# Performance work log

Measured on AMD Instinct MI355X. Metric: run time of the kernel, lower is better.

Reference implementation:

```python
import jax, jax.numpy as jnp
import numpy as np
from jax import lax

LAM = 1.0   # risk.distance calls wasserstein with lam=1
ITS = 20    # and its=20
EPS_K = 1e-6


def setup_inputs() -> dict:
    key = jax.random.key(0)
    k1, k2 = jax.random.split(key)
    N, S, D = 4096, 32, 128
    X_ls = jax.random.normal(k1, (N, S, D), dtype=jnp.float32)
    t = jax.random.randint(k2, (N,), 0, 2).astype(jnp.int32)
    return {"X_ls": X_ls, "t": t}


def _pdist2sq(X, Y):
    # squared Euclidean distance between all pairs: [nt, nc]
    C = -2.0 * (X @ Y.T)
    nx = jnp.sum(jnp.square(X), axis=1, keepdims=True)   # [nt,1]
    ny = jnp.sum(jnp.square(Y), axis=1, keepdims=True)   # [nc,1]
    return C + ny.T + nx


def _sinkhorn_step(Xt, Xc, p, lam, its):
    # Xt: [nt, d], Xc: [nc, d]  -> scalar 2*sum(T*Mt)
    nt = jnp.float32(Xt.shape[0])
    nc = jnp.float32(Xc.shape[0])
    M = _pdist2sq(Xt, Xc)                                   # [nt, nc]
    delta = lax.stop_gradient(jnp.max(M))
    eff_lam = lax.stop_gradient(lam / jnp.mean(M))
    # augmented cost matrix Mt: [nt+1, nc+1]
    row = delta * jnp.ones((1, M.shape[1]), M.dtype)
    col = jnp.concatenate([delta * jnp.ones((M.shape[0], 1), M.dtype),
                           jnp.zeros((1, 1), M.dtype)], axis=0)
    Mt = jnp.concatenate([jnp.concatenate([M, row], axis=0), col], axis=1)
    # marginals a: [nt+1,1], b: [nc+1,1]
    a = jnp.concatenate([(p / nt) * jnp.ones((Xt.shape[0], 1), M.dtype),
                         (1.0 - p) * jnp.ones((1, 1), M.dtype)], axis=0)
    b = jnp.concatenate([((1.0 - p) / nc) * jnp.ones((Xc.shape[0], 1), M.dtype),
                         p * jnp.ones((1, 1), M.dtype)], axis=0)
    K = jnp.exp(-eff_lam * Mt) + EPS_K
    ainvK = K / a
    def body(i, u):
        # u^T K -> transpose -> K^T u : [nc+1,1]
        return 1.0 / (ainvK @ (b / (K.T @ u)))
    u = lax.fori_loop(0, its, body, a)
    v = b / (K.T @ u)                                       # [nc+1,1]
    T = u * (v.T * K)                                       # [nt+1, nc+1]
    T = lax.stop_gradient(T)                                # backpropT=False
    return 2.0 * jnp.sum(T * Mt)


def _wasserstein(X_ls, t, lam=LAM, its=ITS):
    # Data-dependent split on treatment (concrete, eager) — matches tf.where+gather.
    t_np = np.asarray(t)
    it_idx = np.nonzero(t_np > 0)[0]
    ic_idx = np.nonzero(t_np < 1)[0]
    p = jnp.float32(t_np.astype(np.float32).mean())          # p_t = np.mean(t)
    Xt_all = jnp.transpose(X_ls[it_idx], (1, 0, 2))          # [S, nt, d]
    Xc_all = jnp.transpose(X_ls[ic_idx], (1, 0, 2))          # [S, nc, d]
    per_step = jax.vmap(lambda Xt, Xc: _sinkhorn_step(Xt, Xc, p, lam, its))
    return jnp.sum(per_step(Xt_all, Xc_all))                 # sum over timesteps


def reference(X_ls, t):
    return _wasserstein(X_ls, t)
```

## Files before the change

kernel.cpp:

```cpp
#include <hip/hip_runtime.h>
#include <stdint.h>

typedef unsigned char u8;
typedef unsigned short u16;
typedef uint32_t u32;

#define NTOT 4096
#define SS   32
#define DD   128
#define EPSK 1e-6f
#define NITER 20
#define CAPC 4460544u
#define LDC_FIT 2304
#define WSTR 2432
#define SU_OFF 2308
#define UNT_OFF 2309
#define BPT 16

typedef __attribute__((ext_vector_type(8))) short short8;
typedef __attribute__((ext_vector_type(4))) float f32x4;
typedef __attribute__((ext_vector_type(2))) float f32x2;

__device__ __forceinline__ float bf2f(u16 h){ return __uint_as_float(((u32)h) << 16); }
__device__ __forceinline__ u16 f2bf(float f){
  u32 u = __float_as_uint(f);
  u += 0x7fffu + ((u >> 16) & 1u);
  return (u16)(u >> 16);
}
__device__ __forceinline__ int invpermc(int cp){
  return (cp & ~63) | ((cp & 3) << 4) | ((cp >> 2) & 15);
}

__global__ __launch_bounds__(1024) void k_compact(const int* __restrict__ t,
    int* __restrict__ itidx, int* __restrict__ icidx, int* __restrict__ meta,
    float* __restrict__ fmeta)
{
  __shared__ int sc[1024];
  int tid = threadIdx.x;
  int e0 = tid * 4;
  int tv[4]; int c = 0;
  #pragma unroll
  for (int e = 0; e < 4; e++){ tv[e] = t[e0 + e]; c += (tv[e] > 0) ? 1 : 0; }
  sc[tid] = c;
  __syncthreads();
  for (int off = 1; off < 1024; off <<= 1){
    int v = sc[tid];
    int add = (tid >= off) ? sc[tid - off] : 0;
    __syncthreads();
    sc[tid] = v + add;
    __syncthreads();
  }
  int incl = sc[tid];
  int excl = incl - c;
  int oT = excl, oC = e0 - excl;
  #pragma unroll
  for (int e = 0; e < 4; e++){
    if (tv[e] > 0) itidx[oT++] = e0 + e;
    else           icidx[oC++] = e0 + e;
  }
  if (tid == 1023){
    meta[0] = incl; meta[1] = NTOT - incl;
    fmeta[0] = (float)incl / (float)NTOT;
  }
}

__global__ void k_zero(float* __restrict__ p, int n)
{
  int i = blockIdx.x * 256 + threadIdx.x;
  if (i < n) p[i] = 0.f;
}

__global__ void k_vinit(const float* __restrict__ fmeta, float* __restrict__ w0)
{
  if (threadIdx.x == 0){
    float p = fmeta[0];
    float* w = w0 + (size_t)blockIdx.x * WSTR;
    w[SU_OFF]  = p;
    w[UNT_OFF] = 1.0f - p;
  }
}

__global__ __launch_bounds__(256) void k_pack(const float* __restrict__ X,
    const int* __restrict__ itidx, const int* __restrict__ icidx,
    const int* __restrict__ meta, u16* __restrict__ XT, u16* __restrict__ XC,
    float* __restrict__ nxT, float* __restrict__ nxC, int ts0)
{
  int r = blockIdx.x * 256 + threadIdx.x;
  int isC = blockIdx.y;
  int z = blockIdx.z;
  int s = ts0 + z;
  int n = isC ? meta[1] : meta[0];
  if (r >= n) return;
  int idx = isC ? icidx[r] : itidx[r];
  const float4* src = (const float4*)(X + ((size_t)idx * SS + s) * DD);
  u16* dst = (isC ? XC : XT) + ((size_t)z * NTOT + r) * DD;
  float nrm = 0.f;
  #pragma unroll
  for (int q = 0; q < 32; q++){
    float4 v = src[q];
    nrm += v.x*v.x + v.y*v.y + v.z*v.z + v.w*v.w;
    u32 lo = (u32)f2bf(v.x) | ((u32)f2bf(v.y) << 16);
    u32 hi = (u32)f2bf(v.z) | ((u32)f2bf(v.w) << 16);
    uint2 pk; pk.x = lo; pk.y = hi;
    ((uint2*)dst)[q] = pk;
  }
  (isC ? nxC : nxT)[z * NTOT + r] = nrm;
}

__global__ __launch_bounds__(256) void k_stats(const u16* __restrict__ XT,
    const u16* __restrict__ XC, const float* __restrict__ nxT, const float* __restrict__ nxC,
    const int* __restrict__ meta, float* __restrict__ gsx, float* __restrict__ gsn)
{
  int side = blockIdx.y, z = blockIdx.z;
  int n = side ? meta[1] : meta[0];
  int chunk = (n + 7) >> 3;
  int r0 = blockIdx.x * chunk;
  int r1 = min(r0 + chunk, n);
  const u16* B = (side ? XC : XT) + (size_t)z * NTOT * DD;
  int tid = threadIdx.x;
  int d = tid & 127, half = tid >> 7;
  float sx = 0.f;
  for (int r = r0 + half; r < r1; r += 2) sx += bf2f(B[(size_t)r * DD + d]);
  __shared__ float sp[256];
  sp[tid] = sx;
  __syncthreads();
  if (tid < 128) unsafeAtomicAdd(&gsx[(size_t)(z*2+side)*128 + tid], sp[tid] + sp[tid+128]);
  const float* nrm = (side ? nxC : nxT) + (size_t)z * NTOT;
  float sn = 0.f;
  for (int r = r0 + tid; r < r1; r += 256) sn += nrm[r];
  #pragma unroll
  for (int o = 32; o; o >>= 1) sn += __shfl_xor(sn, o);
  __syncthreads();
  if ((tid & 63) == 0) sp[tid >> 6] = sn;
  __syncthreads();
  if (tid == 0) unsafeAtomicAdd(&gsn[z*2+side], sp[0]+sp[1]+sp[2]+sp[3]);
}

__global__ void k_lam(const float* __restrict__ gsx, const float* __restrict__ gsn,
                      const int* __restrict__ meta, float* __restrict__ stats)
{
  int z = blockIdx.x, tid = threadIdx.x;
  float d = gsx[(size_t)(z*2)*128 + tid] * gsx[(size_t)(z*2+1)*128 + tid];
  #pragma unroll
  for (int o = 32; o; o >>= 1) d += __shfl_xor(d, o);
  __shared__ float rr[2];
  if ((tid & 63) == 0) rr[tid >> 6] = d;
  __syncthreads();
  if (tid == 0){
    float nt = (float)meta[0], nc = (float)meta[1];
    float msum = nc * gsn[z*2] + nt * gsn[z*2+1] - 2.f * (rr[0] + rr[1]);
    stats[z*8+0] = nt * nc / msum;
    stats[z*8+1] = msum / (nt * nc);
  }
}

#define LDA2 72
__global__ __launch_bounds__(256) void k_gemm(const u16* __restrict__ XT,
    const u16* __restrict__ XC, const float* __restrict__ nxT, const float* __restrict__ nxC,
    const int* __restrict__ meta, const float* __restrict__ fmeta,
    float* __restrict__ stats, u8* __restrict__ Kc, float* __restrict__ w0base)
{
  int nt = meta[0], nc = meta[1];
  if (nt > LDC_FIT || nc > LDC_FIT) return;
  int bx = blockIdx.x, by = blockIdx.y, z = blockIdx.z;
  if (by * 128 >= nt || bx * 128 >= nc) return;
  __shared__ __align__(16) u16 As[128 * LDA2];
  __shared__ __align__(16) u16 Bs[128 * LDA2];
  __shared__ float watile[256];
  int tid = threadIdx.x;
  int wid = tid >> 6, lane = tid & 63;
  int wm = (wid >> 1) * 64, wn = (wid & 1) * 64;
  int lrow = lane & 15, lquad = lane >> 4;

  f32x4 acc[4][4];
  #pragma unroll
  for (int i = 0; i < 4; i++){
    #pragma unroll
    for (int j = 0; j < 4; j++){
      acc[i][j][0]=0.f; acc[i][j][1]=0.f; acc[i][j][2]=0.f; acc[i][j][3]=0.f;
    }
  }

  int r = tid & 127;
  int isB = tid >> 7;
  int g = (isB ? bx : by) * 128 + r;
  int lim = isB ? nc : nt;
  const u16* srcbase = (isB ? XC : XT) + ((size_t)z * NTOT + g) * DD;
  u16* dl = (isB ? Bs : As) + r * LDA2;

  for (int kh = 0; kh < 2; kh++){
    __syncthreads();
    if (g < lim){
      const uint4* src = (const uint4*)(srcbase + kh * 64);
      #pragma unroll
      for (int q = 0; q < 8; q++) ((uint4*)dl)[q] = src[q];
    } else {
      uint4 zz; zz.x=0; zz.y=0; zz.z=0; zz.w=0;
      #pragma unroll
      for (int q = 0; q < 8; q++) ((uint4*)dl)[q] = zz;
    }
    __syncthreads();
    #pragma unroll
    for (int ks = 0; ks < 2; ks++){
      int koff = ks * 32 + lquad * 8;
      short8 af[4], bfr[4];
      #pragma unroll
      for (int i = 0; i < 4; i++) af[i]  = *(const short8*)(As + (wm + i*16 + lrow) * LDA2 + koff);
      #pragma unroll
      for (int j = 0; j < 4; j++) bfr[j] = *(const short8*)(Bs + (wn + j*16 + lrow) * LDA2 + koff);
      #pragma unroll
      for (int i = 0; i < 4; i++){
        #pragma unroll
        for (int j = 0; j < 4; j++){
          acc[i][j] = __builtin_amdgcn_mfma_f32_16x16x32_bf16(af[i], bfr[j], acc[i][j], 0, 0, 0);
        }
      }
    }
  }

  int ldc = (nc + 127) & ~127;
  float lam = stats[z*8+0];
  float p = fmeta[0];
  float a0 = p / (float)nt;
  const float* nxTr = nxT + (size_t)z * NTOT;
  const float* nxCr = nxC + (size_t)z * NTOT;
  u8* Kz = Kc + (size_t)z * CAPC;

  float nyv[4]; bool jin[4];
  #pragma unroll
  for (int j = 0; j < 4; j++){
    int gj = bx*128 + wn + j*16 + lrow;
    jin[j] = gj < nc;
    nyv[j] = jin[j] ? nxCr[gj] : 0.f;
  }
  float vmax = 0.f;
  float colsum[4] = {0.f, 0.f, 0.f, 0.f};
  size_t cbase = (size_t)(bx*128 + wn + lrow*4);
  #pragma unroll
  for (int i = 0; i < 4; i++){
    #pragma unroll
    for (int rr2 = 0; rr2 < 4; rr2++){
      int gi = by*128 + wm + i*16 + lquad*4 + rr2;
      bool iin = gi < nt;
      float nxv = iin ? nxTr[gi] : 0.f;
      float cv[4];
      #pragma unroll
      for (int j = 0; j < 4; j++){
        float m = nxv + nyv[j] - 2.0f * acc[i][j][rr2];
        cv[j] = __expf(-lam * m);
        if (iin && jin[j]){ vmax = fmaxf(vmax, m); colsum[j] += cv[j]; }
      }
      u32 pk = (u32)__builtin_amdgcn_cvt_pk_fp8_f32(cv[0], cv[1], 0, false);
      pk = (u32)__builtin_amdgcn_cvt_pk_fp8_f32(cv[2], cv[3], (int)pk, true);
      if (iin) *(u32*)(Kz + (size_t)gi * ldc + cbase) = pk;
    }
  }
  #pragma unroll
  for (int j = 0; j < 4; j++){
    colsum[j] += __shfl_xor(colsum[j], 16);
    colsum[j] += __shfl_xor(colsum[j], 32);
  }
  if (lane < 16){
    #pragma unroll
    for (int j = 0; j < 4; j++) watile[wid * 64 + j*16 + lrow] = colsum[j];
  }
  #pragma unroll
  for (int o = 32; o; o >>= 1) vmax = fmaxf(vmax, __shfl_xor(vmax, o));
  if (lane == 0) atomicMax((int*)stats + z*8 + 2, __float_as_int(vmax));
  __syncthreads();
  if (tid < 128){
    int gj = bx*128 + tid;
    if (gj < nc){
      float v = (tid < 64) ? (watile[tid] + watile[128 + tid])
                           : (watile[64 + (tid-64)] + watile[192 + (tid-64)]);
      unsafeAtomicAdd(w0base + (size_t)z * WSTR + gj, v * a0);
    }
  }
}

__global__ __launch_bounds__(256, 2) void k_iter(const u8* __restrict__ Kc,
    const float* __restrict__ wprev, float* __restrict__ wnext,
    float* __restrict__ ubuf, const int* __restrict__ meta,
    const float* __restrict__ fmeta, const float* __restrict__ stats, int writeU)
{
  __shared__ __align__(16) float zl[LDC_FIT];
  __shared__ __align__(16) float watw[4 * LDC_FIT];
  __shared__ float red[4];
  int nt = meta[0], nc = meta[1];
  if (nt > LDC_FIT || nc > LDC_FIT) return;
  int ldc = (nc + 127) & ~127;
  int z = blockIdx.y, b = blockIdx.x;
  int tid = threadIdx.x, wid = tid >> 6, lane = tid & 63;
  float p = fmeta[0];
  float b0 = (1.0f - p) / (float)nc;
  float a0 = p / (float)nt;
  float lam = stats[z*8+0];
  float delta = stats[z*8+2];
  float kc = __expf(-lam * delta);
  float kce = kc + EPSK;
  const float* wp = wprev + (size_t)z * WSTR;
  float* wnx = wnext + (size_t)z * WSTR;
  float SU = wp[SU_OFF], UNT = wp[UNT_OFF];
  float wext = EPSK * (SU + UNT) + kc * UNT;
  float wnc = kce * SU + (1.0f + EPSK) * UNT;
  float znc = p / wnc;

  float zp = 0.f;
  for (int cp = tid; cp < ldc; cp += 256){
    int c = invpermc(cp);
    float v = 0.f;
    if (c < nc) v = b0 * __builtin_amdgcn_rcpf(wp[c] + wext);
    zl[cp] = v;
    zp += v;
  }
  #pragma unroll
  for (int o = 32; o; o >>= 1) zp += __shfl_xor(zp, o);
  if (lane == 0) red[wid] = zp;
  __syncthreads();
  float Z = red[0] + red[1] + red[2] + red[3];
  float dotX = EPSK * Z + kce * znc;
  float untN = (1.0f - p) / (kce * Z + (1.0f + EPSK) * znc);

  int cb0 = lane * 16;
  float zv[48];
  #pragma unroll
  for (int s = 0; s < 3; s++){
    int cb = s*1024 + cb0;
    if (cb < ldc){
      #pragma unroll
      for (int q = 0; q < 4; q++){
        float4 t4 = *(const float4*)(zl + cb + q*4);
        zv[s*16+q*4+0]=t4.x; zv[s*16+q*4+1]=t4.y; zv[s*16+q*4+2]=t4.z; zv[s*16+q*4+3]=t4.w;
      }
    } else {
      #pragma unroll
      for (int k = 0; k < 16; k++) zv[s*16+k] = 0.f;
    }
  }

  float wacc[48];
  #pragma unroll
  for (int k = 0; k < 48; k++) wacc[k] = 0.f;
  float rsum = 0.f;

  int rpb = (nt + BPT - 1) / BPT;
  int r0 = b * rpb, r1 = min(r0 + rpb, nt);
  const u8* Kz = Kc + (size_t)z * CAPC;

  for (int r = r0 + wid; r < r1; r += 4){
    const u8* Kr = Kz + (size_t)r * ldc;
    uint4 kq[3];
    #pragma unroll
    for (int s = 0; s < 3; s++){
      int cb = s*1024 + cb0;
      if (cb < ldc) kq[s] = *(const uint4*)(Kr + cb);
      else { kq[s].x=0u; kq[s].y=0u; kq[s].z=0u; kq[s].w=0u; }
    }
    float kd[48];
    #pragma unroll
    for (int s = 0; s < 3; s++){
      u32 wd[4] = {kq[s].x, kq[s].y, kq[s].z, kq[s].w};
      #pragma unroll
      for (int q = 0; q < 4; q++){
        f32x2 d0 = __builtin_amdgcn_cvt_pk_f32_fp8((int)wd[q], false);
        f32x2 d1 = __builtin_amdgcn_cvt_pk_f32_fp8((int)wd[q], true);
        kd[s*16+q*4+0] = d0.x; kd[s*16+q*4+1] = d0.y;
        kd[s*16+q*4+2] = d1.x; kd[s*16+q*4+3] = d1.y;
      }
    }
    float dot = 0.f;
    #pragma unroll
    for (int k = 0; k < 48; k++) dot = fmaf(kd[k], zv[k], dot);
    #pragma unroll
    for (int o = 32; o; o >>= 1) dot += __shfl_xor(dot, o);
    float uv = a0 * __builtin_amdgcn_rcpf(dot + dotX);
    rsum += uv;
    if (writeU && lane == 0) ubuf[(size_t)z * WSTR + r] = uv;
    #pragma unroll
    for (int k = 0; k < 48; k++) wacc[k] = fmaf(kd[k], uv, wacc[k]);
  }
  #pragma unroll
  for (int s = 0; s < 3; s++){
    int cb = s*1024 + cb0;
    if (cb < ldc){
      #pragma unroll
      for (int q = 0; q < 4; q++)
        *(float4*)(watw + (size_t)wid * LDC_FIT + cb + q*4) =
            make_float4(wacc[s*16+q*4+0], wacc[s*16+q*4+1], wacc[s*16+q*4+2], wacc[s*16+q*4+3]);
    }
  }
  if (lane == 0) unsafeAtomicAdd(wnx + SU_OFF, rsum);
  if (b == 0 && tid == 0) wnx[UNT_OFF] = untN;
  __syncthreads();
  for (int cp = tid; cp < ldc; cp += 256){
    int c = invpermc(cp);
    if (c < nc){
      float v = watw[cp] + watw[LDC_FIT + cp] + watw[2*LDC_FIT + cp] + watw[3*LDC_FIT + cp];
      unsafeAtomicAdd(wnx + c, v);
    }
  }
}

__global__ __launch_bounds__(256, 2) void k_fin(const u8* __restrict__ Kc,
    const float* __restrict__ wprev, const float* __restrict__ ubuf,
    const int* __restrict__ meta, const float* __restrict__ fmeta,
    const float* __restrict__ stats, float* __restrict__ tsacc, int ts0)
{
  __shared__ __align__(16) float zl[LDC_FIT];
  __shared__ float red[4];
  int nt = meta[0], nc = meta[1];
  if (nt > LDC_FIT || nc > LDC_FIT) return;
  int ldc = (nc + 127) & ~127;
  int z = blockIdx.y, b = blockIdx.x;
  int tid = threadIdx.x, wid = tid >> 6, lane = tid & 63;
  float p = fmeta[0];
  float b0 = (1.0f - p) / (float)nc;
  float lam = stats[z*8+0];
  float invlam = stats[z*8+1];
  float delta = stats[z*8+2];
  float kc = __expf(-lam * delta);
  float kce = kc + EPSK;
  const float* wp = wprev + (size_t)z * WSTR;
  float SU = wp[SU_OFF], UNT = wp[UNT_OFF];
  float wext = EPSK * (SU + UNT) + kc * UNT;
  float wnc = kce * SU + (1.0f + EPSK) * UNT;
  float znc = p / wnc;

  float zp = 0.f;
  for (int cp = tid; cp < ldc; cp += 256){
    int c = invpermc(cp);
    float v = 0.f;
    if (c < nc) v = b0 * __builtin_amdgcn_rcpf(wp[c] + wext);
    zl[cp] = v;
    zp += v;
  }
  #pragma unroll
  for (int o = 32; o; o >>= 1) zp += __shfl_xor(zp, o);
  if (lane == 0) red[wid] = zp;
  __syncthreads();
  float Z = red[0] + red[1] + red[2] + red[3];

  int cb0 = lane * 16;
  float zv[48];
  #pragma unroll
  for (int s = 0; s < 3; s++){
    int cb = s*1024 + cb0;
    if (cb < ldc){
      #pragma unroll
      for (int q = 0; q < 4; q++){
        float4 t4 = *(const float4*)(zl + cb + q*4);
        zv[s*16+q*4+0]=t4.x; zv[s*16+q*4+1]=t4.y; zv[s*16+q*4+2]=t4.z; zv[s*16+q*4+3]=t4.w;
      }
    } else {
      #pragma unroll
      for (int k = 0; k < 16; k++) zv[s*16+k] = 0.f;
    }
  }

  int rpb = (nt + BPT - 1) / BPT;
  int r0 = b * rpb, r1 = min(r0 + rpb, nt);
  const u8* Kz = Kc + (size_t)z * CAPC;
  float wsum = 0.f;

  for (int r = r0 + wid; r < r1; r += 4){
    const u8* Kr = Kz + (size_t)r * ldc;
    float inner = 0.f;
    #pragma unroll
    for (int s = 0; s < 3; s++){
      int cb = s*1024 + cb0;
      if (cb < ldc){
        uint4 kq = *(const uint4*)(Kr + cb);
        u32 wd[4] = {kq.x, kq.y, kq.z, kq.w};
        #pragma unroll
        for (int q = 0; q < 4; q++){
          f32x2 d0 = __builtin_amdgcn_cvt_pk_f32_fp8((int)wd[q], false);
          f32x2 d1 = __builtin_amdgcn_cvt_pk_f32_fp8((int)wd[q], true);
          float c0 = d0.x, c1 = d0.y, c2 = d1.x, c3 = d1.y;
          int k0 = s*16+q*4;
          inner += (c0 + EPSK) * zv[k0+0] * __logf(fmaxf(c0, 1e-4f));
          inner += (c1 + EPSK) * zv[k0+1] * __logf(fmaxf(c1, 1e-4f));
          inner += (c2 + EPSK) * zv[k0+2] * __logf(fmaxf(c2, 1e-4f));
          inner += (c3 + EPSK) * zv[k0+3] * __logf(fmaxf(c3, 1e-4f));
        }
      }
    }
    #pragma unroll
    for (int o = 32; o; o >>= 1) inner += __shfl_xor(inner, o);
    wsum += ubuf[(size_t)z * WSTR + r] * inner;
  }
  if (lane == 0) unsafeAtomicAdd(tsacc + ts0 + z, -invlam * wsum);
  if (b == 0 && tid == 0){
    float aug = delta * kce * (UNT * Z + SU * znc);
    unsafeAtomicAdd(tsacc + ts0 + z, aug);
  }
}

__global__ void k_out(const float* __restrict__ tsacc, float* __restrict__ out)
{
  if (threadIdx.x == 0){
    float s = 0.f;
    for (int i = 0; i < SS; i++) s += tsacc[i];
    out[0] = 2.0f * s;
  }
}

extern "C" void kernel_launch(void* const* d_in, const int* in_sizes, int n_in,
                              void* d_out, int out_size, void* d_ws, size_t ws_size,
                              hipStream_t stream)
{
  const float* X = (const float*)d_in[0];
  const int* t = (const int*)d_in[1];

  const size_t PER_TS = 6810000u;
  const size_t FIXED  = 262144u;
  int TSG = 1;
  if (ws_size > FIXED + PER_TS){
    size_t g = (ws_size - FIXED) / PER_TS;
    TSG = (g > SS) ? SS : (int)g;
  }

  char* pp = (char*)d_ws;
  auto alloc = [&](size_t bytes) -> void* {
    void* r = (void*)pp;
    pp += (bytes + 255) & ~(size_t)255;
    return r;
  };
  u8*    Kbuf  = (u8*)alloc((size_t)TSG * CAPC);
  u16*   XT    = (u16*)alloc((size_t)TSG * NTOT * DD * 2);
  u16*   XC    = (u16*)alloc((size_t)TSG * NTOT * DD * 2);
  float* nxT   = (float*)alloc((size_t)TSG * NTOT * 4);
  float* nxC   = (float*)alloc((size_t)TSG * NTOT * 4);
  float* wbuf  = (float*)alloc((size_t)(NITER + 1) * TSG * WSTR * 4);
  float* ubuf  = (float*)alloc((size_t)TSG * WSTR * 4);
  float* auxf  = (float*)alloc((size_t)TSG * 272 * 4);
  int*   itidx = (int*)alloc(NTOT * 4);
  int*   icidx = (int*)alloc(NTOT * 4);
  int*   meta  = (int*)alloc(256);
  float* fmeta = (float*)alloc(256);
  float* tsacc = (float*)alloc(256);

  float* gsx   = auxf;
  float* gsn   = auxf + (size_t)TSG*256;
  float* stats = gsn + (size_t)TSG*2;
  const int auxn = TSG * 266;
  const int wn  = (NITER + 1) * TSG * WSTR;

  k_zero<<<1, 256, 0, stream>>>(tsacc, 64);
  k_compact<<<1, 1024, 0, stream>>>(t, itidx, icidx, meta, fmeta);

  for (int ts0 = 0; ts0 < SS; ts0 += TSG){
    int cnt = SS - ts0; if (cnt > TSG) cnt = TSG;

    k_zero<<<(auxn + 255)/256, 256, 0, stream>>>(auxf, auxn);
    k_zero<<<(wn + 255)/256, 256, 0, stream>>>(wbuf, wn);
    k_vinit<<<cnt, 64, 0, stream>>>(fmeta, wbuf);
    k_pack<<<dim3(16, 2, cnt), 256, 0, stream>>>(X, itidx, icidx, meta, XT, XC, nxT, nxC, ts0);
    k_stats<<<dim3(8, 2, cnt), 256, 0, stream>>>(XT, XC, nxT, nxC, meta, gsx, gsn);
    k_lam<<<cnt, 128, 0, stream>>>(gsx, gsn, meta, stats);
    k_gemm<<<dim3(18, 18, cnt), 256, 0, stream>>>(XT, XC, nxT, nxC, meta, fmeta, stats, Kbuf, wbuf);

    for (int it = 0; it < NITER; it++){
      k_iter<<<dim3(BPT, cnt), 256, 0, stream>>>(Kbuf,
          wbuf + (size_t)it * TSG * WSTR,
          wbuf + (size_t)(it + 1) * TSG * WSTR,
          ubuf, meta, fmeta, stats, (it == NITER - 1) ? 1 : 0);
    }
    k_fin<<<dim3(BPT, cnt), 256, 0, stream>>>(Kbuf,
        wbuf + (size_t)NITER * TSG * WSTR, ubuf, meta, fmeta, stats, tsacc, ts0);
  }
  k_out<<<1, 64, 0, stream>>>(tsacc, (float*)d_out);
}
```

Measured before the change: 1.248 ms.

## Prefetch K rows, cut iter LDS with shared atomics, raise occupancy and grid

The Sinkhorn iteration and final kernels now software-prefetch the next row's fp8 K values while processing the current one. They re-decode K instead of keeping 48 decoded floats live, and split dot products into four accumulators. k_iter replaces its four per-wave LDS partial buffers with a single buffer updated by LDS atomics, which shrinks shared memory so occupancy can rise to 3 blocks per CU. BPT grows from 16 to 24 blocks per timestep. k_gemm stages the norm vectors in LDS and requests 4 blocks per CU. The costs are LDS atomic contention and the extra fp8 decode work.

```diff
diff --git a/kernel.cpp b/kernel.cpp
--- a/kernel.cpp
+++ b/kernel.cpp
@@ -15,7 +15,7 @@
 #define WSTR 2432
 #define SU_OFF 2308
 #define UNT_OFF 2309
-#define BPT 16
+#define BPT 24
 
 typedef __attribute__((ext_vector_type(8))) short short8;
 typedef __attribute__((ext_vector_type(4))) float f32x4;
@@ -29,6 +29,15 @@
 }
 __device__ __forceinline__ int invpermc(int cp){
   return (cp & ~63) | ((cp & 3) << 4) | ((cp >> 2) & 15);
+}
+__device__ __forceinline__ void dec16(uint4 kq, float* kd){
+  u32 wd[4] = {kq.x, kq.y, kq.z, kq.w};
+  #pragma unroll
+  for (int q = 0; q < 4; q++){
+    f32x2 d0 = __builtin_amdgcn_cvt_pk_f32_fp8((int)wd[q], false);
+    f32x2 d1 = __builtin_amdgcn_cvt_pk_f32_fp8((int)wd[q], true);
+    kd[q*4+0] = d0.x; kd[q*4+1] = d0.y; kd[q*4+2] = d1.x; kd[q*4+3] = d1.y;
+  }
 }
 
 __global__ __launch_bounds__(1024) void k_compact(const int* __restrict__ t,
@@ -155,7 +164,7 @@
 }
 
 #define LDA2 72
-__global__ __launch_bounds__(256) void k_gemm(const u16* __restrict__ XT,
+__global__ __launch_bounds__(256, 4) void k_gemm(const u16* __restrict__ XT,
     const u16* __restrict__ XC, const float* __restrict__ nxT, const float* __restrict__ nxC,
     const int* __restrict__ meta, const float* __restrict__ fmeta,
     float* __restrict__ stats, u8* __restrict__ Kc, float* __restrict__ w0base)
@@ -167,10 +176,20 @@
   __shared__ __align__(16) u16 As[128 * LDA2];
   __shared__ __align__(16) u16 Bs[128 * LDA2];
   __shared__ float watile[256];
+  __shared__ float nxs[128];
+  __shared__ float nys[128];
   int tid = threadIdx.x;
   int wid = tid >> 6, lane = tid & 63;
   int wm = (wid >> 1) * 64, wn = (wid & 1) * 64;
   int lrow = lane & 15, lquad = lane >> 4;
+
+  if (tid < 128){
+    int gi = by*128 + tid;
+    nxs[tid] = (gi < nt) ? nxT[(size_t)z * NTOT + gi] : 0.f;
+  } else {
+    int gj = bx*128 + (tid - 128);
+    nys[tid - 128] = (gj < nc) ? nxC[(size_t)z * NTOT + gj] : 0.f;
+  }
 
   f32x4 acc[4][4];
   #pragma unroll
@@ -222,16 +241,14 @@
   float lam = stats[z*8+0];
   float p = fmeta[0];
   float a0 = p / (float)nt;
-  const float* nxTr = nxT + (size_t)z * NTOT;
-  const float* nxCr = nxC + (size_t)z * NTOT;
   u8* Kz = Kc + (size_t)z * CAPC;
 
   float nyv[4]; bool jin[4];
   #pragma unroll
   for (int j = 0; j < 4; j++){
-    int gj = bx*128 + wn + j*16 + lrow;
-    jin[j] = gj < nc;
-    nyv[j] = jin[j] ? nxCr[gj] : 0.f;
+    int lcol = wn + j*16 + lrow;
+    jin[j] = (bx*128 + lcol) < nc;
+    nyv[j] = nys[lcol];
   }
   float vmax = 0.f;
   float colsum[4] = {0.f, 0.f, 0.f, 0.f};
@@ -240,9 +257,10 @@
   for (int i = 0; i < 4; i++){
     #pragma unroll
     for (int rr2 = 0; rr2 < 4; rr2++){
-      int gi = by*128 + wm + i*16 + lquad*4 + rr2;
+      int lr = wm + i*16 + lquad*4 + rr2;
+      int gi = by*128 + lr;
       bool iin = gi < nt;
-      float nxv = iin ? nxTr[gi] : 0.f;
+      float nxv = nxs[lr];
       float cv[4];
       #pragma unroll
       for (int j = 0; j < 4; j++){
@@ -278,13 +296,13 @@
   }
 }
 
-__global__ __launch_bounds__(256, 2) void k_iter(const u8* __restrict__ Kc,
+__global__ __launch_bounds__(256, 3) void k_iter(const u8* __restrict__ Kc,
     const float* __restrict__ wprev, float* __restrict__ wnext,
     float* __restrict__ ubuf, const int* __restrict__ meta,
     const float* __restrict__ fmeta, const float* __restrict__ stats, int writeU)
 {
   __shared__ __align__(16) float zl[LDC_FIT];
-  __shared__ __align__(16) float watw[4 * LDC_FIT];
+  __shared__ float watw[LDC_FIT];
   __shared__ float red[4];
   int nt = meta[0], nc = meta[1];
   if (nt > LDC_FIT || nc > LDC_FIT) return;
@@ -311,6 +329,7 @@
     float v = 0.f;
     if (c < nc) v = b0 * __builtin_amdgcn_rcpf(wp[c] + wext);
     zl[cp] = v;
+    watw[cp] = 0.f;
     zp += v;
   }
   #pragma unroll
@@ -346,47 +365,55 @@
   int rpb = (nt + BPT - 1) / BPT;
   int r0 = b * rpb, r1 = min(r0 + rpb, nt);
   const u8* Kz = Kc + (size_t)z * CAPC;
-
-  for (int r = r0 + wid; r < r1; r += 4){
+  uint4 zq; zq.x=0u; zq.y=0u; zq.z=0u; zq.w=0u;
+
+  int r = r0 + wid;
+  uint4 cur[3] = {zq, zq, zq};
+  if (r < r1){
     const u8* Kr = Kz + (size_t)r * ldc;
-    uint4 kq[3];
+    cur[0] = *(const uint4*)(Kr + cb0);
+    if (1024 + cb0 < ldc) cur[1] = *(const uint4*)(Kr + 1024 + cb0);
+    if (2048 + cb0 < ldc) cur[2] = *(const uint4*)(Kr + 2048 + cb0);
+  }
+  while (r < r1){
+    int rn = r + 4;
+    uint4 nxt[3] = {zq, zq, zq};
+    if (rn < r1){
+      const u8* Krn = Kz + (size_t)rn * ldc;
+      nxt[0] = *(const uint4*)(Krn + cb0);
+      if (1024 + cb0 < ldc) nxt[1] = *(const uint4*)(Krn + 1024 + cb0);
+      if (2048 + cb0 < ldc) nxt[2] = *(const uint4*)(Krn + 2048 + cb0);
+    }
+    float d4[4] = {0.f, 0.f, 0.f, 0.f};
     #pragma unroll
     for (int s = 0; s < 3; s++){
-      int cb = s*1024 + cb0;
-      if (cb < ldc) kq[s] = *(const uint4*)(Kr + cb);
-      else { kq[s].x=0u; kq[s].y=0u; kq[s].z=0u; kq[s].w=0u; }
-    }
-    float kd[48];
-    #pragma unroll
-    for (int s = 0; s < 3; s++){
-      u32 wd[4] = {kq[s].x, kq[s].y, kq[s].z, kq[s].w};
-      #pragma unroll
-      for (int q = 0; q < 4; q++){
-        f32x2 d0 = __builtin_amdgcn_cvt_pk_f32_fp8((int)wd[q], false);
-        f32x2 d1 = __builtin_amdgcn_cvt_pk_f32_fp8((int)wd[q], true);
-        kd[s*16+q*4+0] = d0.x; kd[s*16+q*4+1] = d0.y;
-        kd[s*16+q*4+2] = d1.x; kd[s*16+q*4+3] = d1.y;
-      }
-    }
-    float dot = 0.f;
-    #pragma unroll
-    for (int k = 0; k < 48; k++) dot = fmaf(kd[k], zv[k], dot);
+      float kd[16];
+      dec16(cur[s], kd);
+      #pragma unroll
+      for (int k = 0; k < 16; k++) d4[k & 3] = fmaf(kd[k], zv[s*16+k], d4[k & 3]);
+    }
+    float dot = (d4[0] + d4[1]) + (d4[2] + d4[3]);
     #pragma unroll
     for (int o = 32; o; o >>= 1) dot += __shfl_xor(dot, o);
     float uv = a0 * __builtin_amdgcn_rcpf(dot + dotX);
     rsum += uv;
     if (writeU && lane == 0) ubuf[(size_t)z * WSTR + r] = uv;
     #pragma unroll
-    for (int k = 0; k < 48; k++) wacc[k] = fmaf(kd[k], uv, wacc[k]);
+    for (int s = 0; s < 3; s++){
+      float kd[16];
+      dec16(cur[s], kd);
+      #pragma unroll
+      for (int k = 0; k < 16; k++) wacc[s*16+k] = fmaf(kd[k], uv, wacc[s*16+k]);
+    }
+    cur[0] = nxt[0]; cur[1] = nxt[1]; cur[2] = nxt[2];
+    r = rn;
   }
   #pragma unroll
   for (int s = 0; s < 3; s++){
     int cb = s*1024 + cb0;
     if (cb < ldc){
       #pragma unroll
-      for (int q = 0; q < 4; q++)
-        *(float4*)(watw + (size_t)wid * LDC_FIT + cb + q*4) =
-            make_float4(wacc[s*16+q*4+0], wacc[s*16+q*4+1], wacc[s*16+q*4+2], wacc[s*16+q*4+3]);
+      for (int k = 0; k < 16; k++) atomicAdd(&watw[cb + k], wacc[s*16+k]);
     }
   }
   if (lane == 0) unsafeAtomicAdd(wnx + SU_OFF, rsum);
@@ -394,14 +421,11 @@
   __syncthreads();
   for (int cp = tid; cp < ldc; cp += 256){
     int c = invpermc(cp);
-    if (c < nc){
-      float v = watw[cp] + watw[LDC_FIT + cp] + watw[2*LDC_FIT + cp] + watw[3*LDC_FIT + cp];
-      unsafeAtomicAdd(wnx + c, v);
-    }
-  }
-}
-
-__global__ __launch_bounds__(256, 2) void k_fin(const u8* __restrict__ Kc,
+    if (c < nc) unsafeAtomicAdd(wnx + c, watw[cp]);
+  }
+}
+
+__global__ __launch_bounds__(256, 3) void k_fin(const u8* __restrict__ Kc,
     const float* __restrict__ wprev, const float* __restrict__ ubuf,
     const int* __restrict__ meta, const float* __restrict__ fmeta,
     const float* __restrict__ stats, float* __restrict__ tsacc, int ts0)
@@ -461,32 +485,42 @@
   int r0 = b * rpb, r1 = min(r0 + rpb, nt);
   const u8* Kz = Kc + (size_t)z * CAPC;
   float wsum = 0.f;
-
-  for (int r = r0 + wid; r < r1; r += 4){
+  uint4 zq; zq.x=0u; zq.y=0u; zq.z=0u; zq.w=0u;
+
+  int r = r0 + wid;
+  uint4 cur[3] = {zq, zq, zq};
+  if (r < r1){
     const u8* Kr = Kz + (size_t)r * ldc;
-    float inner = 0.f;
+    cur[0] = *(const uint4*)(Kr + cb0);
+    if (1024 + cb0 < ldc) cur[1] = *(const uint4*)(Kr + 1024 + cb0);
+    if (2048 + cb0 < ldc) cur[2] = *(const uint4*)(Kr + 2048 + cb0);
+  }
+  while (r < r1){
+    int rn = r + 4;
+    uint4 nxt[3] = {zq, zq, zq};
+    if (rn < r1){
+      const u8* Krn = Kz + (size_t)rn * ldc;
+      nxt[0] = *(const uint4*)(Krn + cb0);
+      if (1024 + cb0 < ldc) nxt[1] = *(const uint4*)(Krn + 1024 + cb0);
+      if (2048 + cb0 < ldc) nxt[2] = *(const uint4*)(Krn + 2048 + cb0);
+    }
+    float d4[4] = {0.f, 0.f, 0.f, 0.f};
     #pragma unroll
     for (int s = 0; s < 3; s++){
-      int cb = s*1024 + cb0;
-      if (cb < ldc){
-        uint4 kq = *(const uint4*)(Kr + cb);
-        u32 wd[4] = {kq.x, kq.y, kq.z, kq.w};
-        #pragma unroll
-        for (int q = 0; q < 4; q++){
-          f32x2 d0 = __builtin_amdgcn_cvt_pk_f32_fp8((int)wd[q], false);
-          f32x2 d1 = __builtin_amdgcn_cvt_pk_f32_fp8((int)wd[q], true);
-          float c0 = d0.x, c1 = d0.y, c2 = d1.x, c3 = d1.y;
-          int k0 = s*16+q*4;
-          inner += (c0 + EPSK) * zv[k0+0] * __logf(fmaxf(c0, 1e-4f));
-          inner += (c1 + EPSK) * zv[k0+1] * __logf(fmaxf(c1, 1e-4f));
-          inner += (c2 + EPSK) * zv[k0+2] * __logf(fmaxf(c2, 1e-4f));
-          inner += (c3 + EPSK) * zv[k0+3] * __logf(fmaxf(c3, 1e-4f));
-        }
+      float kd[16];
+      dec16(cur[s], kd);
+      #pragma unroll
+      for (int k = 0; k < 16; k++){
+        float c0 = kd[k];
+        d4[k & 3] = fmaf((c0 + EPSK) * zv[s*16+k], __logf(fmaxf(c0, 1e-4f)), d4[k & 3]);
       }
     }
+    float inner = (d4[0] + d4[1]) + (d4[2] + d4[3]);
     #pragma unroll
     for (int o = 32; o; o >>= 1) inner += __shfl_xor(inner, o);
     wsum += ubuf[(size_t)z * WSTR + r] * inner;
+    cur[0] = nxt[0]; cur[1] = nxt[1]; cur[2] = nxt[2];
+    r = rn;
   }
   if (lane == 0) unsafeAtomicAdd(tsacc + ts0 + z, -invlam * wsum);
   if (b == 0 && tid == 0){
```

After: 2.042 ms. 63.6% more time.
